# Kernel tuning notes

Hardware: AMD Instinct MI355X
Metric: run time of the kernel (lower is better)

The kernel has to match this reference:

```python
import jax, jax.numpy as jnp
import numpy as np

N = 50000
E = 800000
D = 128          # in_channels == hidden_channels
L = 3            # num_layers
JK = D * L       # jk 'cat' output
H2 = D // 2      # classifier hidden
C = 2            # out classes
EPS = 1e-5


def setup_inputs() -> dict:
    key = jax.random.key(0)
    ks = jax.random.split(key, 16)
    x = jax.random.normal(ks[0], (N, D), dtype=jnp.float32)
    edge_index = jax.random.randint(ks[1], (2, E), 0, N, dtype=jnp.int64)
    s = 0.05
    Wl = jax.random.normal(ks[2], (L, D, D), dtype=jnp.float32) * s   # lin_l (on aggregated), has bias
    bl = jax.random.normal(ks[3], (L, D), dtype=jnp.float32) * s
    Wr = jax.random.normal(ks[4], (L, D, D), dtype=jnp.float32) * s   # lin_r (on root), no bias
    gamma = jnp.ones((L, D), dtype=jnp.float32)
    beta = jnp.zeros((L, D), dtype=jnp.float32)
    rmean = jax.random.normal(ks[5], (L, D), dtype=jnp.float32) * s
    rvar = jax.random.uniform(ks[6], (L, D), dtype=jnp.float32, minval=0.5, maxval=1.5)
    Wc1 = jax.random.normal(ks[7], (JK, H2), dtype=jnp.float32) * s
    bc1 = jax.random.normal(ks[8], (H2,), dtype=jnp.float32) * s
    Wc2 = jax.random.normal(ks[9], (H2, C), dtype=jnp.float32) * s
    bc2 = jax.random.normal(ks[10], (C,), dtype=jnp.float32) * s
    return {"x": x, "edge_index": edge_index, "Wl": Wl, "bl": bl, "Wr": Wr,
            "gamma": gamma, "beta": beta, "rmean": rmean, "rvar": rvar,
            "Wc1": Wc1, "bc1": bc1, "Wc2": Wc2, "bc2": bc2}


def reference(x, edge_index, Wl, bl, Wr, gamma, beta, rmean, rvar, Wc1, bc1, Wc2, bc2):
    src, dst = edge_index[0], edge_index[1]
    # node in-degree (for mean aggregation), clamp to avoid div-by-zero
    deg = jax.ops.segment_sum(jnp.ones((E,), dtype=x.dtype), dst, num_segments=N)
    inv_deg = 1.0 / jnp.maximum(deg, 1.0)  # [N]

    h = x
    layer_outputs = []
    for i in range(L):
        # SAGEConv(mean): out = lin_l(mean_{j in N(i)} h_j) + lin_r(h_i)
        agg = jax.ops.segment_sum(h[src], dst, num_segments=N) * inv_deg[:, None]  # [N, D]
        h = agg @ Wl[i] + bl[i] + h @ Wr[i]
        # BatchNorm (eval: running stats), then ReLU; Dropout is identity in eval
        h = (h - rmean[i]) * jax.lax.rsqrt(rvar[i] + EPS) * gamma[i] + beta[i]
        h = jax.nn.relu(h)
        layer_outputs.append(h)

    jk = jnp.concatenate(layer_outputs, axis=-1)  # [N, L*D]
    z = jax.nn.relu(jk @ Wc1 + bc1)
    logits = z @ Wc2 + bc2  # [N, 2]
    return logits
```

## Files before the change

kernel.cpp:

```cpp
#include <hip/hip_runtime.h>
#include <hip/hip_fp16.h>
#include <cstdint>
#include <cstddef>

#define DD 128
#define JKD 384
#define EPSV 1e-5f
#define BSH 7
#define NBMAX 512
#define BCAP2 4096
#define PCH 8192
#define PTH 1024
#define BCAP 8192

typedef __attribute__((ext_vector_type(8))) short bf16x8;
typedef __attribute__((ext_vector_type(4))) float f32x4;
#define MFMA(a, b, c) __builtin_amdgcn_mfma_f32_16x16x32_bf16(a, b, c, 0, 0, 0)

__device__ inline unsigned short f2bf_rne(float f) {
  unsigned u = __float_as_uint(f);
  unsigned r = u + 0x7fffu + ((u >> 16) & 1u);
  return (unsigned short)(r >> 16);
}

__device__ inline void split8(const float* s, bf16x8& hi, bf16x8& lo) {
#pragma unroll
  for (int j = 0; j < 8; ++j) {
    float f = s[j];
    unsigned short h = f2bf_rne(f);
    float fh = __uint_as_float((unsigned)h << 16);
    hi[j] = (short)h;
    lo[j] = (short)f2bf_rne(f - fh);
  }
}

__device__ inline void h8_to_f8(uint4 raw, float* out) {
  const __half2* hp = reinterpret_cast<const __half2*>(&raw);
#pragma unroll
  for (int j = 0; j < 4; ++j) {
    float2 f = __half22float2(hp[j]);
    out[2 * j] = f.x;
    out[2 * j + 1] = f.y;
  }
}

__device__ __forceinline__ void gload16(const void* g, void* l) {
  __builtin_amdgcn_global_load_lds(
      (const __attribute__((address_space(1))) unsigned int*)g,
      (__attribute__((address_space(3))) unsigned int*)l, 16, 0, 0);
}

__global__ void init_cursor(int* __restrict__ cursor) {
  int t = threadIdx.x;
  if (t < NBMAX) cursor[t] = t * BCAP2;
}

__global__ __launch_bounds__(PTH) void partition_prep(
    const int* __restrict__ src, const int* __restrict__ dst, int* bucket_cursor,
    unsigned* __restrict__ packed, int E, int nChunks,
    const float* __restrict__ Wl, const float* __restrict__ Wr, bf16x8* __restrict__ wf,
    const float* __restrict__ Wc1, bf16x8* __restrict__ wcf,
    const float* __restrict__ x, unsigned short* __restrict__ x16, int N) {
  __shared__ int h[NBMAX];
  __shared__ int lofs[NBMAX];
  __shared__ int res[NBMAX];
  __shared__ int lcur[NBMAX];
  __shared__ int wsum[4];
  __shared__ int wpref[4];
  __shared__ unsigned stage[PCH];

  if (blockIdx.x < nChunks) {
    int t = threadIdx.x;
    int lane = t & 63;
    int base = blockIdx.x * PCH;
    for (int i = t; i < NBMAX; i += PTH) h[i] = 0;
    __syncthreads();
#pragma unroll
    for (int it = 0; it < PCH / PTH; ++it) {
      int e = base + it * PTH + t;
      if (e < E) {
        int d = __builtin_nontemporal_load(dst + e);
        atomicAdd(&h[d >> BSH], 1);
      }
    }
    __syncthreads();
    int c0 = 0, c1 = 0, s = 0, sc = 0;
    if (t < 256) {
      c0 = h[2 * t];
      c1 = h[2 * t + 1];
      s = c0 + c1;
      sc = s;
#pragma unroll
      for (int off = 1; off < 64; off <<= 1) {
        int u = __shfl_up(sc, off, 64);
        if (lane >= off) sc += u;
      }
      if (lane == 63) wsum[t >> 6] = sc;
    }
    __syncthreads();
    if (t == 0) {
      int a = 0;
#pragma unroll
      for (int w = 0; w < 4; ++w) { wpref[w] = a; a += wsum[w]; }
    }
    __syncthreads();
    if (t < 256) {
      int excl = wpref[t >> 6] + sc - s;
      lofs[2 * t] = excl;
      lofs[2 * t + 1] = excl + c0;
      lcur[2 * t] = excl;
      lcur[2 * t + 1] = excl + c0;
      if (c0 > 0) res[2 * t] = atomicAdd(&bucket_cursor[2 * t], c0);
      if (c1 > 0) res[2 * t + 1] = atomicAdd(&bucket_cursor[2 * t + 1], c1);
    }
    __syncthreads();
#pragma unroll
    for (int it = 0; it < PCH / PTH; ++it) {
      int e = base + it * PTH + t;
      if (e < E) {
        int d = __builtin_nontemporal_load(dst + e);
        int sv = __builtin_nontemporal_load(src + e);
        int pos = atomicAdd(&lcur[d >> BSH], 1);
        stage[pos] = ((unsigned)(d & ((1 << BSH) - 1)) << 16) | (unsigned)(sv & 0xffff);
      }
    }
    __syncthreads();
    int wid = t >> 6;
    for (int b = wid; b < NBMAX; b += PTH / 64) {
      int run = h[b];
      if (run == 0) continue;
      int gbase = res[b], lbase = lofs[b];
      for (int j = lane; j < run; j += 64) packed[gbase + j] = stage[lbase + j];
    }
  } else {
    int sub = threadIdx.x >> 8;
    int t = threadIdx.x & 255;
    int f16blocks = (N * 16 + 255) / 256;
    int vb = (blockIdx.x - nChunks) * 4 + sub;
    if (vb >= 60 + f16blocks) return;
    if (vb < 48) {
      int idx = vb * 256 + t;
      int ln = idx & 63;
      int ksnt = (idx >> 6) & 31;
      int mat = (idx >> 11) & 1;
      int layer = idx >> 12;
      int ks = ksnt >> 3, nt = ksnt & 7;
      int nn = nt * 16 + (ln & 15);
      int k0 = ks * 32 + (ln >> 4) * 8;
      const float* W = (mat ? Wr : Wl) + (size_t)layer * DD * DD;
      float v[8];
#pragma unroll
      for (int j = 0; j < 8; ++j) v[j] = W[(size_t)(k0 + j) * DD + nn];
      bf16x8 hi, lo;
      split8(v, hi, lo);
      size_t base = (size_t)((layer * 2 + mat) * 2) * 2048 + (size_t)ksnt * 64 + ln;
      wf[base] = hi;
      wf[base + 2048] = lo;
    } else if (vb < 60) {
      int idx = (vb - 48) * 256 + t;
      int ln = idx & 63;
      int ksnt = idx >> 6;
      int ks = ksnt >> 2, nt = ksnt & 3;
      int nn = nt * 16 + (ln & 15);
      int k0 = ks * 32 + (ln >> 4) * 8;
      float v[8];
#pragma unroll
      for (int j = 0; j < 8; ++j) v[j] = Wc1[(size_t)(k0 + j) * 64 + nn];
      bf16x8 hi, lo;
      split8(v, hi, lo);
      wcf[idx] = hi;
      wcf[idx + 3072] = lo;
    } else {
      int idx = (vb - 60) * 256 + t;
      int r = idx >> 4, cc = (idx & 15) * 8;
      if (r < N) {
        const float* p = x + (size_t)r * DD + cc;
        float4 a = *reinterpret_cast<const float4*>(p);
        float4 bb = *reinterpret_cast<const float4*>(p + 4);
        __half2 h0 = __floats2half2_rn(a.x, a.y);
        __half2 h1 = __floats2half2_rn(a.z, a.w);
        __half2 h2 = __floats2half2_rn(bb.x, bb.y);
        __half2 h3 = __floats2half2_rn(bb.z, bb.w);
        uint4 o;
        o.x = *reinterpret_cast<unsigned*>(&h0);
        o.y = *reinterpret_cast<unsigned*>(&h1);
        o.z = *reinterpret_cast<unsigned*>(&h2);
        o.w = *reinterpret_cast<unsigned*>(&h3);
        *reinterpret_cast<uint4*>(x16 + (size_t)r * DD + cc) = o;
      }
    }
  }
}

__global__ __launch_bounds__(256) void csr_build(const unsigned* __restrict__ packed,
                                                 const int* __restrict__ bucket_cursor,
                                                 int* __restrict__ row_start,
                                                 int* __restrict__ row_end,
                                                 float* __restrict__ inv_deg,
                                                 unsigned short* __restrict__ col, int N) {
  __shared__ int cntA[128];
  __shared__ int lcur[128];
  __shared__ int wsum2[2];
  __shared__ int wpref2[2];
  __shared__ unsigned short stage[BCAP];
  int t = threadIdx.x;
  int b = blockIdx.x;
  int s0 = b * BCAP2;
  int cnt = bucket_cursor[b] - s0;
  if (t < 128) cntA[t] = 0;
  __syncthreads();
  for (int i = t; i < cnt; i += 256) {
    unsigned p = packed[s0 + i];
    atomicAdd(&cntA[p >> 16], 1);
  }
  __syncthreads();
  if (t < 128) {
    int lane = t & 63, wid = t >> 6;
    int v = cntA[t];
    int sc = v;
#pragma unroll
    for (int off = 1; off < 64; off <<= 1) {
      int u = __shfl_up(sc, off, 64);
      if (lane >= off) sc += u;
    }
    if (lane == 63) wsum2[wid] = sc;
    __syncthreads();
    if (t == 0) { wpref2[0] = 0; wpref2[1] = wsum2[0]; }
    __syncthreads();
    int excl = wpref2[wid] + sc - v;
    lcur[t] = excl;
    int node = b * 128 + t;
    if (node < N) {
      row_start[node] = s0 + excl;
      row_end[node] = s0 + excl + v;
      inv_deg[node] = 1.0f / fmaxf((float)v, 1.0f);
    }
  } else {
    __syncthreads();
    __syncthreads();
  }
  __syncthreads();
  for (int i = t; i < cnt; i += 256) {
    unsigned p = packed[s0 + i];
    int pos = atomicAdd(&lcur[p >> 16], 1);
    unsigned short us = (unsigned short)(p & 0xffff);
    if (pos < BCAP) stage[pos] = us;
    else col[s0 + pos] = us;
  }
  __syncthreads();
  int lim = min(cnt, BCAP);
  for (int i = t; i < lim; i += 256) col[s0 + i] = stage[i];
}

__global__ __launch_bounds__(256) void agg16_kernel(const unsigned short* __restrict__ h16,
                                                    int ldh,
                                                    const int* __restrict__ row_start,
                                                    const int* __restrict__ row_end,
                                                    const unsigned short* __restrict__ col,
                                                    const float* __restrict__ inv_deg,
                                                    unsigned short* __restrict__ agg16, int n) {
  int wib = threadIdx.x >> 6;
  int lane = threadIdx.x & 63;
  int node = blockIdx.x * 4 + wib;
  if (node >= n) return;
  int beg = row_start[node];
  int end = row_end[node];
  float ax = 0.f, ay = 0.f;

  for (int j0 = beg; j0 < end; j0 += 64) {
    int cnt = end - j0;
    if (cnt > 64) cnt = 64;
    int cv = (int)col[j0 + min(lane, cnt - 1)];
#pragma unroll 1
    for (int e0 = 0; e0 < cnt; e0 += 8) {
      int ce = cnt - e0;
      if (ce > 8) ce = 8;
      unsigned u[8];
#pragma unroll
      for (int k = 0; k < 8; ++k) {
        int e = e0 + k;
        int s = __shfl(cv, e < cnt ? e : 0);
        if (k < ce) u[k] = *reinterpret_cast<const unsigned*>(h16 + (size_t)s * ldh + lane * 2);
      }
#pragma unroll
      for (int k = 0; k < 8; ++k) {
        if (k < ce) {
          float2 f = __half22float2(*reinterpret_cast<__half2*>(&u[k]));
          ax += f.x;
          ay += f.y;
        }
      }
    }
  }
  float wd = inv_deg[node];
  __half2 hv = __floats2half2_rn(ax * wd, ay * wd);
  *reinterpret_cast<unsigned*>(agg16 + (size_t)node * DD + lane * 2) =
      *reinterpret_cast<unsigned*>(&hv);
}

__global__ __launch_bounds__(256) void layer_gemm_mfma(
    const unsigned short* __restrict__ hin16, int ldh,
    const unsigned short* __restrict__ agg16,
    const bf16x8* __restrict__ Blh_g, const bf16x8* __restrict__ Bll_g,
    const bf16x8* __restrict__ Brh_g, const bf16x8* __restrict__ Brl_g,
    const float* __restrict__ bl, const float* __restrict__ gamma,
    const float* __restrict__ beta, const float* __restrict__ rmean,
    const float* __restrict__ rvar, unsigned short* __restrict__ out16, int n) {
  __shared__ __align__(16) unsigned char smem[32768];
  int t = threadIdx.x;
  int w = t >> 6, lane = t & 63;
  int lane16 = lane & 15, quad = lane >> 4;
  int row0 = blockIdx.x * 64;
  int m = row0 + w * 16 + lane16;
  bool valid = m < n;
  size_t mrow = (size_t)(valid ? m : 0);
  const unsigned short* ap = agg16 + mrow * DD + quad * 8;
  const unsigned short* hp = hin16 + mrow * (size_t)ldh + quad * 8;

  const bf16x8* halfp = (w == 0) ? Blh_g : (w == 1) ? Bll_g : (w == 2) ? Brh_g : Brl_g;
  unsigned char* sreg = smem + w * 8192;

#pragma unroll
  for (int c = 0; c < 8; ++c) gload16(halfp + c * 64 + lane, sreg + c * 1024);

  bf16x8 Ah[4], Al[4], Hh[4], Hl[4];
#pragma unroll
  for (int ks = 0; ks < 4; ++ks) {
    float a8[8], h8[8];
    if (valid) {
      uint4 ra = *reinterpret_cast<const uint4*>(ap + ks * 32);
      uint4 rh = *reinterpret_cast<const uint4*>(hp + ks * 32);
      h8_to_f8(ra, a8);
      h8_to_f8(rh, h8);
    } else {
#pragma unroll
      for (int j = 0; j < 8; ++j) { a8[j] = 0.f; h8[j] = 0.f; }
    }
    split8(a8, Ah[ks], Al[ks]);
    split8(h8, Hh[ks], Hl[ks]);
  }

  f32x4 acc[8];
#pragma unroll
  for (int nt = 0; nt < 8; ++nt) acc[nt] = (f32x4){0.f, 0.f, 0.f, 0.f};

  const bf16x8* sB = reinterpret_cast<const bf16x8*>(smem);
  __syncthreads();

#pragma unroll
  for (int ks = 0; ks < 4; ++ks) {
    bf16x8 B0[8], B1[8];
#pragma unroll
    for (int nt = 0; nt < 8; ++nt) B0[nt] = sB[nt * 64 + lane];
#pragma unroll
    for (int nt = 0; nt < 8; ++nt) acc[nt] = MFMA(Ah[ks], B0[nt], acc[nt]);
#pragma unroll
    for (int nt = 0; nt < 8; ++nt) B1[nt] = sB[512 + nt * 64 + lane];
#pragma unroll
    for (int nt = 0; nt < 8; ++nt) acc[nt] = MFMA(Al[ks], B0[nt], acc[nt]);
#pragma unroll
    for (int nt = 0; nt < 8; ++nt) acc[nt] = MFMA(Ah[ks], B1[nt], acc[nt]);
#pragma unroll
    for (int nt = 0; nt < 8; ++nt) B0[nt] = sB[1024 + nt * 64 + lane];
#pragma unroll
    for (int nt = 0; nt < 8; ++nt) acc[nt] = MFMA(Hh[ks], B0[nt], acc[nt]);
#pragma unroll
    for (int nt = 0; nt < 8; ++nt) B1[nt] = sB[1536 + nt * 64 + lane];
#pragma unroll
    for (int nt = 0; nt < 8; ++nt) acc[nt] = MFMA(Hl[ks], B0[nt], acc[nt]);
#pragma unroll
    for (int nt = 0; nt < 8; ++nt) acc[nt] = MFMA(Hh[ks], B1[nt], acc[nt]);
    if (ks < 3) {
      __syncthreads();
#pragma unroll
      for (int c = 0; c < 8; ++c)
        gload16(halfp + (ks + 1) * 512 + c * 64 + lane, sreg + c * 1024);
      __syncthreads();
    }
  }

#pragma unroll
  for (int nt = 0; nt < 8; ++nt) {
    int c = nt * 16 + lane16;
    float sc = gamma[c] * rsqrtf(rvar[c] + EPSV);
    float sh = (bl[c] - rmean[c]) * sc + beta[c];
#pragma unroll
    for (int r = 0; r < 4; ++r) {
      int orow = row0 + w * 16 + quad * 4 + r;
      if (orow < n) {
        float v = fmaxf(fmaf(acc[nt][r], sc, sh), 0.f);
        __half hv = __float2half_rn(v);
        out16[(size_t)orow * JKD + c] = *reinterpret_cast<unsigned short*>(&hv);
      }
    }
  }
}

__global__ __launch_bounds__(256) void gemm2_cls(
    const unsigned short* __restrict__ gsrc, int ldg,
    const unsigned short* __restrict__ agg16,
    const bf16x8* __restrict__ Blh_g, const bf16x8* __restrict__ Bll_g,
    const bf16x8* __restrict__ Brh_g, const bf16x8* __restrict__ Brl_g,
    const float* __restrict__ bl, const float* __restrict__ gamma,
    const float* __restrict__ beta, const float* __restrict__ rmean,
    const float* __restrict__ rvar,
    const unsigned short* __restrict__ jk16, const bf16x8* __restrict__ wcf,
    const float* __restrict__ bc1, const float* __restrict__ Wc2,
    const float* __restrict__ bc2, float* __restrict__ out, int n) {
  __shared__ __align__(16) unsigned char smem[17408 + 24576];
  unsigned short (*sOut)[16][136] = reinterpret_cast<unsigned short(*)[16][136]>(smem);
  float (*sZ)[65] = reinterpret_cast<float(*)[65]>(smem);
  unsigned char* clsw = smem + 17408;
  const bf16x8* sB = reinterpret_cast<const bf16x8*>(smem);
  const bf16x8* csB = reinterpret_cast<const bf16x8*>(clsw);
  int t = threadIdx.x;
  int w = t >> 6, lane = t & 63;
  int lane16 = lane & 15, quad = lane >> 4;
  int row0 = blockIdx.x * 64;
  int m = row0 + w * 16 + lane16;
  bool valid = m < n;
  size_t mrow = (size_t)(valid ? m : 0);
  const unsigned short* ap = agg16 + mrow * DD + quad * 8;
  const unsigned short* hp = gsrc + mrow * (size_t)ldg + quad * 8;

  const bf16x8* halfp = (w == 0) ? Blh_g : (w == 1) ? Bll_g : (w == 2) ? Brh_g : Brl_g;
  unsigned char* sreg = smem + w * 8192;

#pragma unroll
  for (int c = 0; c < 8; ++c) gload16(halfp + c * 64 + lane, sreg + c * 1024);

  bf16x8 Ah[4], Al[4], Hh[4], Hl[4];
#pragma unroll
  for (int ks = 0; ks < 4; ++ks) {
    float a8[8], h8[8];
    if (valid) {
      uint4 ra = *reinterpret_cast<const uint4*>(ap + ks * 32);
      uint4 rh = *reinterpret_cast<const uint4*>(hp + ks * 32);
      h8_to_f8(ra, a8);
      h8_to_f8(rh, h8);
    } else {
#pragma unroll
      for (int j = 0; j < 8; ++j) { a8[j] = 0.f; h8[j] = 0.f; }
    }
    split8(a8, Ah[ks], Al[ks]);
    split8(h8, Hh[ks], Hl[ks]);
  }

  f32x4 acc[8];
#pragma unroll
  for (int nt = 0; nt < 8; ++nt) acc[nt] = (f32x4){0.f, 0.f, 0.f, 0.f};

  __syncthreads();

#pragma unroll
  for (int ks = 0; ks < 4; ++ks) {
    bf16x8 B0[8], B1[8];
#pragma unroll
    for (int nt = 0; nt < 8; ++nt) B0[nt] = sB[nt * 64 + lane];
#pragma unroll
    for (int nt = 0; nt < 8; ++nt) acc[nt] = MFMA(Ah[ks], B0[nt], acc[nt]);
#pragma unroll
    for (int nt = 0; nt < 8; ++nt) B1[nt] = sB[512 + nt * 64 + lane];
#pragma unroll
    for (int nt = 0; nt < 8; ++nt) acc[nt] = MFMA(Al[ks], B0[nt], acc[nt]);
#pragma unroll
    for (int nt = 0; nt < 8; ++nt) acc[nt] = MFMA(Ah[ks], B1[nt], acc[nt]);
#pragma unroll
    for (int nt = 0; nt < 8; ++nt) B0[nt] = sB[1024 + nt * 64 + lane];
#pragma unroll
    for (int nt = 0; nt < 8; ++nt) acc[nt] = MFMA(Hh[ks], B0[nt], acc[nt]);
#pragma unroll
    for (int nt = 0; nt < 8; ++nt) B1[nt] = sB[1536 + nt * 64 + lane];
#pragma unroll
    for (int nt = 0; nt < 8; ++nt) acc[nt] = MFMA(Hl[ks], B0[nt], acc[nt]);
#pragma unroll
    for (int nt = 0; nt < 8; ++nt) acc[nt] = MFMA(Hh[ks], B1[nt], acc[nt]);
    if (ks < 3) {
      __syncthreads();
#pragma unroll
      for (int c = 0; c < 8; ++c)
        gload16(halfp + (ks + 1) * 512 + c * 64 + lane, sreg + c * 1024);
      __syncthreads();
    }
  }
  __syncthreads();

#pragma unroll
  for (int nt = 0; nt < 8; ++nt) {
    int c = nt * 16 + lane16;
    float sc = gamma[c] * rsqrtf(rvar[c] + EPSV);
    float sh = (bl[c] - rmean[c]) * sc + beta[c];
#pragma unroll
    for (int r = 0; r < 4; ++r) {
      float v = fmaxf(fmaf(acc[nt][r], sc, sh), 0.f);
      __half hv = __float2half_rn(v);
      sOut[w][quad * 4 + r][c] = *reinterpret_cast<unsigned short*>(&hv);
    }
  }

  const unsigned short* jp = jk16 + mrow * JKD + quad * 8;
  f32x4 cacc[4];
#pragma unroll
  for (int nt = 0; nt < 4; ++nt) cacc[nt] = (f32x4){0.f, 0.f, 0.f, 0.f};

#pragma unroll
  for (int g = 0; g < 4; ++g) {
    __syncthreads();
#pragma unroll
    for (int c = 0; c < 6; ++c) {
      int ch = w * 6 + c;
      const bf16x8* gp = (ch < 12) ? (wcf + g * 768 + ch * 64)
                                   : (wcf + 3072 + g * 768 + (ch - 12) * 64);
      gload16(gp + lane, clsw + ch * 1024);
    }
    __syncthreads();
#pragma unroll
    for (int k3 = 0; k3 < 3; ++k3) {
      int ks = g * 3 + k3;
      float a8[8];
      if (ks < 8) {
        if (valid) {
          uint4 raw = *reinterpret_cast<const uint4*>(jp + ks * 32);
          h8_to_f8(raw, a8);
        } else {
#pragma unroll
          for (int j = 0; j < 8; ++j) a8[j] = 0.f;
        }
      } else {
        uint4 raw = *reinterpret_cast<const uint4*>(&sOut[w][lane16][(ks - 8) * 32 + quad * 8]);
        h8_to_f8(raw, a8);
      }
      bf16x8 Jh, Jl;
      split8(a8, Jh, Jl);
      bf16x8 B0[4], B1[4];
#pragma unroll
      for (int nt = 0; nt < 4; ++nt) B0[nt] = csB[k3 * 256 + nt * 64 + lane];
#pragma unroll
      for (int nt = 0; nt < 4; ++nt) cacc[nt] = MFMA(Jh, B0[nt], cacc[nt]);
#pragma unroll
      for (int nt = 0; nt < 4; ++nt) B1[nt] = csB[768 + k3 * 256 + nt * 64 + lane];
#pragma unroll
      for (int nt = 0; nt < 4; ++nt) cacc[nt] = MFMA(Jl, B0[nt], cacc[nt]);
#pragma unroll
      for (int nt = 0; nt < 4; ++nt) cacc[nt] = MFMA(Jh, B1[nt], cacc[nt]);
    }
  }
  __syncthreads();

#pragma unroll
  for (int nt = 0; nt < 4; ++nt) {
    int c = nt * 16 + lane16;
    float b1 = bc1[c];
#pragma unroll
    for (int r = 0; r < 4; ++r)
      sZ[w * 16 + quad * 4 + r][c] = fmaxf(cacc[nt][r] + b1, 0.f);
  }
  __syncthreads();

  if (t < 128) {
    int r = t >> 1, j = t & 1;
    int gr = row0 + r;
    if (gr < n) {
      float s = bc2[j];
#pragma unroll
      for (int c = 0; c < 64; ++c) s = fmaf(sZ[r][c], Wc2[c * 2 + j], s);
      out[(size_t)gr * 2 + j] = s;
    }
  }
}


extern "C" void kernel_launch(void* const* d_in, const int* in_sizes, int n_in,
                              void* d_out, int out_size, void* d_ws, size_t ws_size,
                              hipStream_t stream) {
  const float* x = (const float*)d_in[0];
  const int* ei = (const int*)d_in[1];
  const float* Wl = (const float*)d_in[2];
  const float* bl = (const float*)d_in[3];
  const float* Wr = (const float*)d_in[4];
  const float* gamma = (const float*)d_in[5];
  const float* beta = (const float*)d_in[6];
  const float* rmean = (const float*)d_in[7];
  const float* rvar = (const float*)d_in[8];
  const float* Wc1 = (const float*)d_in[9];
  const float* bc1 = (const float*)d_in[10];
  const float* Wc2 = (const float*)d_in[11];
  const float* bc2 = (const float*)d_in[12];
  float* out = (float*)d_out;

  const int N = in_sizes[0] / DD;
  const int E = in_sizes[1] / 2;
  const int* src = ei;
  const int* dst = ei + E;

  auto align = [](size_t v) { return (v + 255) & ~(size_t)255; };
  char* ws = (char*)d_ws;
  size_t off = 0;
  int* row_start = (int*)(ws + off);  off = align(off + sizeof(int) * (size_t)N);
  int* row_end = (int*)(ws + off);    off = align(off + sizeof(int) * (size_t)N);
  unsigned short* col = (unsigned short*)(ws + off); off = align(off + sizeof(short) * (size_t)NBMAX * BCAP2);
  float* inv_deg = (float*)(ws + off); off = align(off + sizeof(float) * (size_t)N);
  unsigned* packed = (unsigned*)(ws + off); off = align(off + sizeof(unsigned) * (size_t)NBMAX * BCAP2);
  int* bucket_cursor = (int*)(ws + off); off = align(off + sizeof(int) * NBMAX);
  unsigned short* x16 = (unsigned short*)(ws + off);   off = align(off + sizeof(short) * (size_t)N * DD);
  unsigned short* agg16 = (unsigned short*)(ws + off); off = align(off + sizeof(short) * (size_t)N * DD);
  unsigned short* jk16 = (unsigned short*)(ws + off);  off = align(off + sizeof(short) * (size_t)N * JKD);
  bf16x8* wf = (bf16x8*)(ws + off);  off = align(off + (size_t)16 * 3 * 2 * 2 * 2048);
  bf16x8* wcf = (bf16x8*)(ws + off); off = align(off + (size_t)16 * 2 * 3072);

  const int nbuck = (N + 127) >> BSH;
  const int nChunks = (E + PCH - 1) / PCH;
  int f16blocks = (N * 16 + 255) / 256;
  int prepBlocks = (60 + f16blocks + 3) / 4;

  init_cursor<<<1, NBMAX, 0, stream>>>(bucket_cursor);
  partition_prep<<<nChunks + prepBlocks, PTH, 0, stream>>>(
      src, dst, bucket_cursor, packed, E, nChunks, Wl, Wr, wf, Wc1, wcf, x, x16, N);
  csr_build<<<nbuck, 256, 0, stream>>>(packed, bucket_cursor, row_start, row_end, inv_deg, col, N);

  int nTiles = (N + 63) / 64;
  for (int i = 0; i < 3; ++i) {
    const unsigned short* gsrc = (i == 0) ? x16 : (jk16 + (size_t)(i - 1) * DD);
    int ldg = (i == 0) ? DD : JKD;
    agg16_kernel<<<(N + 3) / 4, 256, 0, stream>>>(gsrc, ldg, row_start, row_end, col, inv_deg, agg16, N);
    bf16x8* Wlf = wf + (size_t)(i * 2 + 0) * 2 * 2048;
    bf16x8* Wrf = wf + (size_t)(i * 2 + 1) * 2 * 2048;
    if (i < 2) {
      layer_gemm_mfma<<<nTiles, 256, 0, stream>>>(
          gsrc, ldg, agg16, Wlf, Wlf + 2048, Wrf, Wrf + 2048,
          bl + (size_t)i * DD, gamma + (size_t)i * DD, beta + (size_t)i * DD,
          rmean + (size_t)i * DD, rvar + (size_t)i * DD, jk16 + (size_t)i * DD, N);
    } else {
      gemm2_cls<<<nTiles, 256, 0, stream>>>(
          gsrc, ldg, agg16, Wlf, Wlf + 2048, Wrf, Wrf + 2048,
          bl + (size_t)i * DD, gamma + (size_t)i * DD, beta + (size_t)i * DD,
          rmean + (size_t)i * DD, rvar + (size_t)i * DD,
          jk16, wcf, bc1, Wc2, bc2, out, N);
    }
  }
}
```

Baseline: 290.7 us.

## Split feature aggregation into two half-width passes with 16-bit lanes

The gather-mean kernel now launches twice as many blocks, and each block covers one 64-column half of the feature row. Each lane loads a single 16-bit value instead of a 32-bit pair. The column indices and output stores also use nontemporal hints. The aim is more parallelism and better cache locality per pass, at the cost of reading the CSR indices twice and issuing narrower, less efficient 128-byte gathers per row.

```diff
diff --git a/kernel.cpp b/kernel.cpp
--- a/kernel.cpp
+++ b/kernel.cpp
@@ -252,50 +252,50 @@
   for (int i = t; i < lim; i += 256) col[s0 + i] = stage[i];
 }
 
-__global__ __launch_bounds__(256) void agg16_kernel(const unsigned short* __restrict__ h16,
-                                                    int ldh,
-                                                    const int* __restrict__ row_start,
-                                                    const int* __restrict__ row_end,
-                                                    const unsigned short* __restrict__ col,
-                                                    const float* __restrict__ inv_deg,
-                                                    unsigned short* __restrict__ agg16, int n) {
+__global__ __launch_bounds__(256) void agg_half_kernel(
+    const unsigned short* __restrict__ h16, int ldh,
+    const int* __restrict__ row_start, const int* __restrict__ row_end,
+    const unsigned short* __restrict__ col, const float* __restrict__ inv_deg,
+    unsigned short* __restrict__ agg16, int n, int nblk) {
   int wib = threadIdx.x >> 6;
   int lane = threadIdx.x & 63;
-  int node = blockIdx.x * 4 + wib;
+  int bid = blockIdx.x;
+  int pass = (bid >= nblk) ? 1 : 0;
+  int node = (bid - pass * nblk) * 4 + wib;
   if (node >= n) return;
   int beg = row_start[node];
   int end = row_end[node];
-  float ax = 0.f, ay = 0.f;
+  const unsigned short* hsrc = h16 + pass * 64 + lane;
+  float a = 0.f;
 
   for (int j0 = beg; j0 < end; j0 += 64) {
     int cnt = end - j0;
     if (cnt > 64) cnt = 64;
-    int cv = (int)col[j0 + min(lane, cnt - 1)];
+    int cv = (int)__builtin_nontemporal_load(col + j0 + min(lane, cnt - 1));
 #pragma unroll 1
     for (int e0 = 0; e0 < cnt; e0 += 8) {
       int ce = cnt - e0;
       if (ce > 8) ce = 8;
-      unsigned u[8];
+      unsigned short u[8];
 #pragma unroll
       for (int k = 0; k < 8; ++k) {
         int e = e0 + k;
         int s = __shfl(cv, e < cnt ? e : 0);
-        if (k < ce) u[k] = *reinterpret_cast<const unsigned*>(h16 + (size_t)s * ldh + lane * 2);
+        if (k < ce) u[k] = hsrc[(size_t)s * ldh];
       }
 #pragma unroll
       for (int k = 0; k < 8; ++k) {
         if (k < ce) {
-          float2 f = __half22float2(*reinterpret_cast<__half2*>(&u[k]));
-          ax += f.x;
-          ay += f.y;
+          __half hh = *reinterpret_cast<__half*>(&u[k]);
+          a += __half2float(hh);
         }
       }
     }
   }
   float wd = inv_deg[node];
-  __half2 hv = __floats2half2_rn(ax * wd, ay * wd);
-  *reinterpret_cast<unsigned*>(agg16 + (size_t)node * DD + lane * 2) =
-      *reinterpret_cast<unsigned*>(&hv);
+  __half hv = __float2half_rn(a * wd);
+  __builtin_nontemporal_store(*reinterpret_cast<unsigned short*>(&hv),
+                              agg16 + (size_t)node * DD + pass * 64 + lane);
 }
 
 __global__ __launch_bounds__(256) void layer_gemm_mfma(
@@ -619,10 +619,12 @@
   csr_build<<<nbuck, 256, 0, stream>>>(packed, bucket_cursor, row_start, row_end, inv_deg, col, N);
 
   int nTiles = (N + 63) / 64;
+  int nblk4 = (N + 3) / 4;
   for (int i = 0; i < 3; ++i) {
     const unsigned short* gsrc = (i == 0) ? x16 : (jk16 + (size_t)(i - 1) * DD);
     int ldg = (i == 0) ? DD : JKD;
-    agg16_kernel<<<(N + 3) / 4, 256, 0, stream>>>(gsrc, ldg, row_start, row_end, col, inv_deg, agg16, N);
+    agg_half_kernel<<<2 * nblk4, 256, 0, stream>>>(gsrc, ldg, row_start, row_end, col,
+                                                   inv_deg, agg16, N, nblk4);
     bf16x8* Wlf = wf + (size_t)(i * 2 + 0) * 2 * 2048;
     bf16x8* Wrf = wf + (size_t)(i * 2 + 1) * 2 * 2048;
     if (i < 2) {
```

New measurement: 512.0 us. +76.1%, slower.
